# Kernel tuning notes

Hardware: AMD Instinct MI355X
Metric: run time of the kernel (lower is better)

The kernel has to match this reference:

```python
import jax, jax.numpy as jnp
import numpy as np

N = 100000   # nodes
E = 1600000  # edges per snapshot
S = 4        # snapshots
D = 128      # node_dim
H = 256      # hidden dim
P = 10000    # post nodes


def setup_inputs() -> dict:
    key = jax.random.key(0)
    ks = jax.random.split(key, 11)
    return {
        "node_features": jax.random.normal(ks[0], (N, D), jnp.float32),
        "edge_index": jax.random.randint(ks[1], (S, 2, E), 0, N, dtype=jnp.int32),
        "post_idx": jax.random.randint(ks[2], (P,), 0, N, dtype=jnp.int32),
        "W1": jax.random.normal(ks[3], (D, H), jnp.float32) * (1.0 / np.sqrt(D)),
        "b1": jnp.zeros((H,), jnp.float32),
        "W2": jax.random.normal(ks[4], (H, H), jnp.float32) * (1.0 / np.sqrt(H)),
        "b2": jnp.zeros((H,), jnp.float32),
        "Wc1": jax.random.normal(ks[5], (H, H // 2), jnp.float32) * (1.0 / np.sqrt(H)),
        "bc1": jnp.zeros((H // 2,), jnp.float32),
        "Wc2": jax.random.normal(ks[6], (H // 2, 1), jnp.float32) * (1.0 / np.sqrt(H // 2)),
        "bc2": jnp.zeros((1,), jnp.float32),
    }


def _gcn_conv(x, W, b, src, dst):
    # PyG GCNConv: linear transform, then symmetric-normalized aggregation
    # with self-loops: out_i = sum_j (xW)_j / sqrt(d_i d_j) + (xW)_i / d_i + b
    xw = x @ W                                   # [N, H]
    deg = jnp.ones((N,), xw.dtype).at[dst].add(1.0)  # in-degree + self-loop
    dinv = jax.lax.rsqrt(deg)                    # [N]
    norm = dinv[src] * dinv[dst]                 # [E]
    msg = xw[src] * norm[:, None]                # [E, H] gather + scale
    agg = jax.ops.segment_sum(msg, dst, num_segments=N)  # scatter-add
    agg = agg + xw * (dinv * dinv)[:, None]      # self-loop term
    return agg + b


def reference(node_features, edge_index, post_idx, W1, b1, W2, b2, Wc1, bc1, Wc2, bc2):
    embs = []
    for s in range(S):  # small fixed snapshot loop
        src, dst = edge_index[s, 0], edge_index[s, 1]
        # layer 0: 128->256, relu (dropout identity in eval), no residual (dim change)
        h = jax.nn.relu(_gcn_conv(node_features, W1, b1, src, dst))
        # layer 1 (last): no relu, residual since dims match
        h = _gcn_conv(h, W2, b2, src, dst) + h
        embs.append(h)
    agg = jnp.mean(jnp.stack(embs), axis=0)      # 'mean' snapshot aggregation
    post = agg[post_idx]                         # [P, H]
    hid = jax.nn.relu(post @ Wc1 + bc1)
    logits = (hid @ Wc2 + bc2)[:, 0]
    return jax.nn.sigmoid(logits)
```

## Files before the change

### kernel.cpp

```cpp
#include <hip/hip_runtime.h>
#include <math.h>

#define N_NODES 100000
#define E_EDGES 1600000
#define S_SNAP  4
#define D_IN    128
#define H_DIM   256
#define P_POST  10000
#define N4 (S_SNAP * N_NODES)
#define E4 (S_SNAP * E_EDGES)
#define NBLK4 ((N4 + 1023) / 1024)
#define NBIN 8
#define BIN_W (N_NODES / NBIN)
#define FILL_CHUNK 2048
#define FILL_NCHUNK ((E4 + FILL_CHUNK - 1) / FILL_CHUNK)

typedef __attribute__((ext_vector_type(8))) short bf16x8;
typedef __attribute__((ext_vector_type(4))) float f32x4;

__device__ __forceinline__ float bf2f(unsigned short u) {
    union { unsigned int i; float f; } v; v.i = ((unsigned int)u) << 16; return v.f;
}
__device__ __forceinline__ unsigned short f2bf(float f) {
    union { float f; unsigned int i; } v; v.f = f;
    unsigned int lsb = (v.i >> 16) & 1u;
    v.i += 0x7fffu + lsb;
    return (unsigned short)(v.i >> 16);
}

__global__ void zero32_kernel(unsigned int* __restrict__ p, int n) {
    int i = blockIdx.x * blockDim.x + threadIdx.x;
    if (i < n) p[i] = 0u;
}

__global__ void hist4_kernel(const int* __restrict__ ei, int* __restrict__ deg4,
        int* __restrict__ slot4) {
    int i = blockIdx.x * 256 + threadIdx.x;
    int s = i / E_EDGES;
    int j = i - s * E_EDGES;
    int d = ei[(size_t)s * 2 * E_EDGES + E_EDGES + j];
    slot4[i] = atomicAdd(&deg4[s * N_NODES + d], 1);
}

__global__ __launch_bounds__(256) void scan_part4_kernel(const int* __restrict__ deg4,
        int* __restrict__ bsum, float* __restrict__ dinv4) {
    __shared__ int red[4];
    int base = blockIdx.x * 1024 + threadIdx.x * 4;
    int4 v = make_int4(0, 0, 0, 0);
    if (base < N4) {
        v = *(const int4*)(deg4 + base);
        dinv4[base + 0] = rsqrtf((float)(v.x + 1));
        dinv4[base + 1] = rsqrtf((float)(v.y + 1));
        dinv4[base + 2] = rsqrtf((float)(v.z + 1));
        dinv4[base + 3] = rsqrtf((float)(v.w + 1));
    }
    int t = v.x + v.y + v.z + v.w;
    #pragma unroll
    for (int off = 32; off > 0; off >>= 1) t += __shfl_down(t, off, 64);
    int wave = threadIdx.x >> 6, lane = threadIdx.x & 63;
    if (lane == 0) red[wave] = t;
    __syncthreads();
    if (threadIdx.x == 0) bsum[blockIdx.x] = red[0] + red[1] + red[2] + red[3];
}

__global__ __launch_bounds__(512) void scan_top_kernel(const int* __restrict__ bsum,
        int* __restrict__ boff) {
    __shared__ int s[512];
    int t = threadIdx.x;
    s[t] = (t < NBLK4) ? bsum[t] : 0;
    __syncthreads();
    for (int off = 1; off < 512; off <<= 1) {
        int v = (t >= off) ? s[t - off] : 0;
        __syncthreads();
        s[t] += v;
        __syncthreads();
    }
    if (t < NBLK4) boff[t] = (t == 0) ? 0 : s[t - 1];
}

__global__ __launch_bounds__(256) void scan_fin4_kernel(const int* __restrict__ deg4,
        const int* __restrict__ boff, int* __restrict__ rowptr4) {
    __shared__ int sh[256];
    int base = blockIdx.x * 1024 + threadIdx.x * 4;
    int4 v = make_int4(0, 0, 0, 0);
    if (base < N4) v = *(const int4*)(deg4 + base);
    int tsum = v.x + v.y + v.z + v.w;
    sh[threadIdx.x] = tsum;
    __syncthreads();
    for (int off = 1; off < 256; off <<= 1) {
        int u = (threadIdx.x >= off) ? sh[threadIdx.x - off] : 0;
        __syncthreads();
        sh[threadIdx.x] += u;
        __syncthreads();
    }
    int excl = boff[blockIdx.x] + sh[threadIdx.x] - tsum;
    if (base < N4) {
        int4 o;
        o.x = excl;
        o.y = excl + v.x;
        o.z = excl + v.x + v.y;
        o.w = excl + v.x + v.y + v.z;
        *(int4*)(rowptr4 + base) = o;
    }
    if (base == 0) rowptr4[N4] = E4;
}

__global__ __launch_bounds__(256) void fill4_kernel(const int* __restrict__ ei,
        const int* __restrict__ slot4, const int* __restrict__ rowptr4,
        int* __restrict__ csrsrc4) {
    int chunk = blockIdx.x >> 3;
    int bin = blockIdx.x & (NBIN - 1);
    int lo = bin * BIN_W, hi = lo + BIN_W;
    int base = chunk * FILL_CHUNK + threadIdx.x;
    #pragma unroll
    for (int k = 0; k < FILL_CHUNK / 256; ++k) {
        int i = base + k * 256;
        if (i < E4) {
            int s = i / E_EDGES;
            int j = i - s * E_EDGES;
            int d = ei[(size_t)s * 2 * E_EDGES + E_EDGES + j];
            if (d >= lo && d < hi) {
                int sc = ei[(size_t)s * 2 * E_EDGES + j];
                csrsrc4[rowptr4[s * N_NODES + d] + slot4[i]] = sc;
            }
        }
    }
}

__global__ __launch_bounds__(256) void gemm_xw1_mfma(const float* __restrict__ A,
        const float* __restrict__ B, unsigned short* __restrict__ C, int M) {
    __shared__ unsigned short As[64][136];
    __shared__ unsigned short Bs[64][136];
    int tid = threadIdx.x;
    int m0 = blockIdx.x * 64, n0 = blockIdx.y * 64;
    {
        int row = tid >> 2, c0 = (tid & 3) * 32;
        int gm = m0 + row;
        #pragma unroll
        for (int i = 0; i < 8; ++i) {
            float4 v = make_float4(0.f, 0.f, 0.f, 0.f);
            if (gm < M) v = *(const float4*)(A + (size_t)gm * D_IN + c0 + i * 4);
            As[row][c0 + i * 4 + 0] = f2bf(v.x);
            As[row][c0 + i * 4 + 1] = f2bf(v.y);
            As[row][c0 + i * 4 + 2] = f2bf(v.z);
            As[row][c0 + i * 4 + 3] = f2bf(v.w);
        }
    }
    {
        int k = tid >> 1, nb = (tid & 1) * 32;
        #pragma unroll
        for (int i = 0; i < 8; ++i) {
            float4 v = *(const float4*)(B + (size_t)k * H_DIM + n0 + nb + i * 4);
            Bs[nb + i * 4 + 0][k] = f2bf(v.x);
            Bs[nb + i * 4 + 1][k] = f2bf(v.y);
            Bs[nb + i * 4 + 2][k] = f2bf(v.z);
            Bs[nb + i * 4 + 3][k] = f2bf(v.w);
        }
    }
    __syncthreads();
    int w = tid >> 6, l = tid & 63;
    int q = l >> 4, mrow = l & 15;
    f32x4 acc[4] = {{0.f,0.f,0.f,0.f},{0.f,0.f,0.f,0.f},{0.f,0.f,0.f,0.f},{0.f,0.f,0.f,0.f}};
    #pragma unroll
    for (int kk = 0; kk < 4; ++kk) {
        bf16x8 a = *(const bf16x8*)&As[16 * w + mrow][kk * 32 + q * 8];
        #pragma unroll
        for (int ct = 0; ct < 4; ++ct) {
            bf16x8 b = *(const bf16x8*)&Bs[ct * 16 + mrow][kk * 32 + q * 8];
            acc[ct] = __builtin_amdgcn_mfma_f32_16x16x32_bf16(a, b, acc[ct], 0, 0, 0);
        }
    }
    #pragma unroll
    for (int ct = 0; ct < 4; ++ct) {
        int col = n0 + ct * 16 + mrow;
        #pragma unroll
        for (int i = 0; i < 4; ++i) {
            int m = m0 + 16 * w + q * 4 + i;
            if (m < M) C[(size_t)m * H_DIM + col] = f2bf(acc[ct][i]);
        }
    }
}

__global__ __launch_bounds__(256) void spmm_l0_kernel(const unsigned short* __restrict__ xw1,
        const float* __restrict__ dinv4, const int* __restrict__ rowptr4,
        const int* __restrict__ csrsrc4, const float* __restrict__ b1,
        unsigned short* __restrict__ h, int soff) {
    int r = (blockIdx.x << 2) + (threadIdx.x >> 6);
    int lane = threadIdx.x & 63;
    int rg = soff + r;
    int e0 = rowptr4[rg], e1 = rowptr4[rg + 1];
    float di = dinv4[rg];
    float4 acc = make_float4(0.f, 0.f, 0.f, 0.f);
    const ushort4* tp = (const ushort4*)xw1;
    const float* dv = dinv4 + soff;
    int e = e0;
    for (; e + 4 <= e1; e += 4) {
        int s0 = csrsrc4[e], s1 = csrsrc4[e + 1], s2 = csrsrc4[e + 2], s3 = csrsrc4[e + 3];
        float w0 = dv[s0] * di, w1 = dv[s1] * di, w2 = dv[s2] * di, w3 = dv[s3] * di;
        ushort4 u0 = tp[(size_t)s0 * 64 + lane];
        ushort4 u1 = tp[(size_t)s1 * 64 + lane];
        ushort4 u2 = tp[(size_t)s2 * 64 + lane];
        ushort4 u3 = tp[(size_t)s3 * 64 + lane];
        acc.x = fmaf(bf2f(u0.x), w0, acc.x); acc.y = fmaf(bf2f(u0.y), w0, acc.y);
        acc.z = fmaf(bf2f(u0.z), w0, acc.z); acc.w = fmaf(bf2f(u0.w), w0, acc.w);
        acc.x = fmaf(bf2f(u1.x), w1, acc.x); acc.y = fmaf(bf2f(u1.y), w1, acc.y);
        acc.z = fmaf(bf2f(u1.z), w1, acc.z); acc.w = fmaf(bf2f(u1.w), w1, acc.w);
        acc.x = fmaf(bf2f(u2.x), w2, acc.x); acc.y = fmaf(bf2f(u2.y), w2, acc.y);
        acc.z = fmaf(bf2f(u2.z), w2, acc.z); acc.w = fmaf(bf2f(u2.w), w2, acc.w);
        acc.x = fmaf(bf2f(u3.x), w3, acc.x); acc.y = fmaf(bf2f(u3.y), w3, acc.y);
        acc.z = fmaf(bf2f(u3.z), w3, acc.z); acc.w = fmaf(bf2f(u3.w), w3, acc.w);
    }
    for (; e < e1; ++e) {
        int s = csrsrc4[e];
        float wv = dv[s] * di;
        ushort4 u = tp[(size_t)s * 64 + lane];
        acc.x = fmaf(bf2f(u.x), wv, acc.x); acc.y = fmaf(bf2f(u.y), wv, acc.y);
        acc.z = fmaf(bf2f(u.z), wv, acc.z); acc.w = fmaf(bf2f(u.w), wv, acc.w);
    }
    ushort4 us = tp[(size_t)r * 64 + lane];
    float wd = di * di;
    float4 bb = ((const float4*)b1)[lane];
    ushort4 o;
    o.x = f2bf(fmaxf(fmaf(bf2f(us.x), wd, acc.x) + bb.x, 0.f));
    o.y = f2bf(fmaxf(fmaf(bf2f(us.y), wd, acc.y) + bb.y, 0.f));
    o.z = f2bf(fmaxf(fmaf(bf2f(us.z), wd, acc.z) + bb.z, 0.f));
    o.w = f2bf(fmaxf(fmaf(bf2f(us.w), wd, acc.w) + bb.w, 0.f));
    ((ushort4*)h)[(size_t)r * 64 + lane] = o;
}

__global__ __launch_bounds__(256) void spmm_h_post_kernel(const unsigned short* __restrict__ h,
        const float* __restrict__ dinv4, const int* __restrict__ rowptr4,
        const int* __restrict__ csrsrc4, const int* __restrict__ post,
        float* __restrict__ t1p, int soff) {
    int p = (blockIdx.x << 2) + (threadIdx.x >> 6);
    int lane = threadIdx.x & 63;
    int r = post[p];
    int rg = soff + r;
    int e0 = rowptr4[rg], e1 = rowptr4[rg + 1];
    float di = dinv4[rg];
    float4 acc = make_float4(0.f, 0.f, 0.f, 0.f);
    const ushort4* hp = (const ushort4*)h;
    const float* dv = dinv4 + soff;
    int e = e0;
    for (; e + 4 <= e1; e += 4) {
        int s0 = csrsrc4[e], s1 = csrsrc4[e + 1], s2 = csrsrc4[e + 2], s3 = csrsrc4[e + 3];
        float w0 = dv[s0] * di, w1 = dv[s1] * di, w2 = dv[s2] * di, w3 = dv[s3] * di;
        ushort4 u0 = hp[(size_t)s0 * 64 + lane];
        ushort4 u1 = hp[(size_t)s1 * 64 + lane];
        ushort4 u2 = hp[(size_t)s2 * 64 + lane];
        ushort4 u3 = hp[(size_t)s3 * 64 + lane];
        acc.x = fmaf(bf2f(u0.x), w0, acc.x); acc.y = fmaf(bf2f(u0.y), w0, acc.y);
        acc.z = fmaf(bf2f(u0.z), w0, acc.z); acc.w = fmaf(bf2f(u0.w), w0, acc.w);
        acc.x = fmaf(bf2f(u1.x), w1, acc.x); acc.y = fmaf(bf2f(u1.y), w1, acc.y);
        acc.z = fmaf(bf2f(u1.z), w1, acc.z); acc.w = fmaf(bf2f(u1.w), w1, acc.w);
        acc.x = fmaf(bf2f(u2.x), w2, acc.x); acc.y = fmaf(bf2f(u2.y), w2, acc.y);
        acc.z = fmaf(bf2f(u2.z), w2, acc.z); acc.w = fmaf(bf2f(u2.w), w2, acc.w);
        acc.x = fmaf(bf2f(u3.x), w3, acc.x); acc.y = fmaf(bf2f(u3.y), w3, acc.y);
        acc.z = fmaf(bf2f(u3.z), w3, acc.z); acc.w = fmaf(bf2f(u3.w), w3, acc.w);
    }
    for (; e < e1; ++e) {
        int s = csrsrc4[e];
        float wv = dv[s] * di;
        ushort4 u = hp[(size_t)s * 64 + lane];
        acc.x = fmaf(bf2f(u.x), wv, acc.x); acc.y = fmaf(bf2f(u.y), wv, acc.y);
        acc.z = fmaf(bf2f(u.z), wv, acc.z); acc.w = fmaf(bf2f(u.w), wv, acc.w);
    }
    ushort4 u = hp[(size_t)r * 64 + lane];
    float wd = di * di;
    acc.x = fmaf(bf2f(u.x), wd, acc.x);
    acc.y = fmaf(bf2f(u.y), wd, acc.y);
    acc.z = fmaf(bf2f(u.z), wd, acc.z);
    acc.w = fmaf(bf2f(u.w), wd, acc.w);
    ((float4*)t1p)[(size_t)p * 64 + lane] = acc;
}

__global__ __launch_bounds__(256) void gemm_l1_mfma(const float* __restrict__ A,
        const float* __restrict__ B, const float* __restrict__ b2,
        const unsigned short* __restrict__ h, const int* __restrict__ post,
        float* __restrict__ accP, int M) {
    __shared__ unsigned short As[64][136];
    __shared__ unsigned short Bs[64][136];
    int tid = threadIdx.x;
    int m0 = blockIdx.x * 64, n0 = blockIdx.y * 64;
    int w = tid >> 6, l = tid & 63;
    int q = l >> 4, mrow = l & 15;
    f32x4 acc[4] = {{0.f,0.f,0.f,0.f},{0.f,0.f,0.f,0.f},{0.f,0.f,0.f,0.f},{0.f,0.f,0.f,0.f}};
    for (int kk = 0; kk < 256; kk += 128) {
        __syncthreads();
        {
            int row = tid >> 2, c0 = (tid & 3) * 32;
            int gm = m0 + row;
            #pragma unroll
            for (int i = 0; i < 8; ++i) {
                float4 v = make_float4(0.f, 0.f, 0.f, 0.f);
                if (gm < M) v = *(const float4*)(A + (size_t)gm * 256 + kk + c0 + i * 4);
                As[row][c0 + i * 4 + 0] = f2bf(v.x);
                As[row][c0 + i * 4 + 1] = f2bf(v.y);
                As[row][c0 + i * 4 + 2] = f2bf(v.z);
                As[row][c0 + i * 4 + 3] = f2bf(v.w);
            }
        }
        {
            int k = tid >> 1, nb = (tid & 1) * 32;
            #pragma unroll
            for (int i = 0; i < 8; ++i) {
                float4 v = *(const float4*)(B + (size_t)(kk + k) * H_DIM + n0 + nb + i * 4);
                Bs[nb + i * 4 + 0][k] = f2bf(v.x);
                Bs[nb + i * 4 + 1][k] = f2bf(v.y);
                Bs[nb + i * 4 + 2][k] = f2bf(v.z);
                Bs[nb + i * 4 + 3][k] = f2bf(v.w);
            }
        }
        __syncthreads();
        #pragma unroll
        for (int ks = 0; ks < 4; ++ks) {
            bf16x8 a = *(const bf16x8*)&As[16 * w + mrow][ks * 32 + q * 8];
            #pragma unroll
            for (int ct = 0; ct < 4; ++ct) {
                bf16x8 b = *(const bf16x8*)&Bs[ct * 16 + mrow][ks * 32 + q * 8];
                acc[ct] = __builtin_amdgcn_mfma_f32_16x16x32_bf16(a, b, acc[ct], 0, 0, 0);
            }
        }
    }
    #pragma unroll
    for (int ct = 0; ct < 4; ++ct) {
        int col = n0 + ct * 16 + mrow;
        float bias = b2[col];
        #pragma unroll
        for (int i = 0; i < 4; ++i) {
            int m = m0 + 16 * w + q * 4 + i;
            if (m < M) {
                int node = post[m];
                float hv = bf2f(h[(size_t)node * 256 + col]);
                accP[(size_t)m * 256 + col] += acc[ct][i] + bias + hv;
            }
        }
    }
}

__global__ __launch_bounds__(128) void classifier_kernel(const float* __restrict__ accP,
        const float* __restrict__ Wc1, const float* __restrict__ bc1,
        const float* __restrict__ Wc2, const float* __restrict__ bc2,
        float* __restrict__ out) {
    __shared__ float arow[8][256];
    __shared__ float red[2][8];
    int p0 = blockIdx.x << 3;
    int tid = threadIdx.x;
    for (int idx = tid; idx < 8 * 256; idx += 128) {
        int pl = idx >> 8, k = idx & 255;
        arow[pl][k] = 0.25f * accP[(size_t)(p0 + pl) * 256 + k];
    }
    __syncthreads();
    float s[8];
    float b = bc1[tid];
    #pragma unroll
    for (int pl = 0; pl < 8; ++pl) s[pl] = b;
    for (int k = 0; k < 256; ++k) {
        float wv = Wc1[k * 128 + tid];
        #pragma unroll
        for (int pl = 0; pl < 8; ++pl) s[pl] = fmaf(arow[pl][k], wv, s[pl]);
    }
    float wc2 = Wc2[tid];
    float part[8];
    #pragma unroll
    for (int pl = 0; pl < 8; ++pl) part[pl] = fmaxf(s[pl], 0.f) * wc2;
    #pragma unroll
    for (int off = 32; off > 0; off >>= 1)
        #pragma unroll
        for (int pl = 0; pl < 8; ++pl) part[pl] += __shfl_down(part[pl], off, 64);
    int wave = tid >> 6, lane = tid & 63;
    if (lane == 0) {
        #pragma unroll
        for (int pl = 0; pl < 8; ++pl) red[wave][pl] = part[pl];
    }
    __syncthreads();
    if (tid < 8) {
        float logit = red[0][tid] + red[1][tid] + bc2[0];
        out[p0 + tid] = 1.f / (1.f + expf(-logit));
    }
}

extern "C" void kernel_launch(void* const* d_in, const int* in_sizes, int n_in,
                              void* d_out, int out_size, void* d_ws, size_t ws_size,
                              hipStream_t stream) {
    const float* x   = (const float*)d_in[0];
    const int*   ei  = (const int*)d_in[1];
    const int*   post= (const int*)d_in[2];
    const float* W1  = (const float*)d_in[3];
    const float* b1  = (const float*)d_in[4];
    const float* W2  = (const float*)d_in[5];
    const float* b2  = (const float*)d_in[6];
    const float* Wc1 = (const float*)d_in[7];
    const float* bc1 = (const float*)d_in[8];
    const float* Wc2 = (const float*)d_in[9];
    const float* bc2 = (const float*)d_in[10];
    float* out = (float*)d_out;

    char* w = (char*)d_ws;
    size_t off = 0;
#define WS_ALLOC(type, name, count) \
    type* name = (type*)(w + off); \
    off += (((size_t)(count) * sizeof(type)) + 255) & ~(size_t)255;
    WS_ALLOC(unsigned short, xw1,     (size_t)N_NODES * H_DIM)
    WS_ALLOC(unsigned short, hbuf,    (size_t)N_NODES * H_DIM)
    WS_ALLOC(float,          t1p,     (size_t)P_POST * H_DIM)
    WS_ALLOC(float,          accP,    (size_t)P_POST * H_DIM)
    WS_ALLOC(int,            deg4,    N4)
    WS_ALLOC(float,          dinv4,   N4)
    WS_ALLOC(int,            rowptr4, N4 + 4)
    WS_ALLOC(int,            csrsrc4, E4)
    WS_ALLOC(int,            bsum,    NBLK4)
    WS_ALLOC(int,            boff,    NBLK4)
#undef WS_ALLOC
    int* slot4 = (int*)hbuf;
    (void)ws_size; (void)in_sizes; (void)n_in; (void)out_size;

    zero32_kernel<<<(P_POST * H_DIM + N4 + 255) / 256, 256, 0, stream>>>(
        (unsigned int*)accP, P_POST * H_DIM + N4);

    hist4_kernel<<<E4 / 256, 256, 0, stream>>>(ei, deg4, slot4);
    scan_part4_kernel<<<NBLK4, 256, 0, stream>>>(deg4, bsum, dinv4);
    scan_top_kernel<<<1, 512, 0, stream>>>(bsum, boff);
    scan_fin4_kernel<<<NBLK4, 256, 0, stream>>>(deg4, boff, rowptr4);
    fill4_kernel<<<FILL_NCHUNK * NBIN, 256, 0, stream>>>(ei, slot4, rowptr4, csrsrc4);

    dim3 gg((N_NODES + 63) / 64, H_DIM / 64);
    gemm_xw1_mfma<<<gg, 256, 0, stream>>>(x, W1, xw1, N_NODES);

    for (int s = 0; s < S_SNAP; ++s) {
        int soff = s * N_NODES;
        spmm_l0_kernel<<<N_NODES / 4, 256, 0, stream>>>(xw1, dinv4, rowptr4, csrsrc4,
                                                        b1, hbuf, soff);
        spmm_h_post_kernel<<<P_POST / 4, 256, 0, stream>>>(hbuf, dinv4, rowptr4, csrsrc4,
                                                           post, t1p, soff);
        dim3 g1((P_POST + 63) / 64, H_DIM / 64);
        gemm_l1_mfma<<<g1, 256, 0, stream>>>(t1p, W2, b2, hbuf, post, accP, P_POST);
    }
    classifier_kernel<<<P_POST / 8, 128, 0, stream>>>(accP, Wc1, bc1, Wc2, bc2, out);
}
```

Before: 1.295 ms.

## Build CSR with per-bin LDS histograms and chunk prefix instead of global atomics

Replaces the global-atomic degree histogram and per-edge slot array with block-local shared-memory counting per (snapshot, destination bin, edge chunk), followed by a per-row prefix over chunks to produce degrees and chunk offsets. The fill kernel then recomputes local slots with LDS atomics and writes source ids at rowptr + chunk offset + local slot. The aim is to remove contended global atomics and the slot array traffic. In exchange, each block rescans its whole edge chunk for every bin (8x more reads of dst), and CSR order within a row is no longer deterministic.

```diff
diff --git a/kernel.cpp b/kernel.cpp
--- a/kernel.cpp
+++ b/kernel.cpp
@@ -12,8 +12,10 @@
 #define NBLK4 ((N4 + 1023) / 1024)
 #define NBIN 8
 #define BIN_W (N_NODES / NBIN)
-#define FILL_CHUNK 2048
-#define FILL_NCHUNK ((E4 + FILL_CHUNK - 1) / FILL_CHUNK)
+#define C_CHUNK 16
+#define EPC (E_EDGES / C_CHUNK)
+#define PREP_BLOCKS (S_SNAP * NBIN * C_CHUNK)
+#define ROWS_PER_BLK (BIN_W / 4)
 
 typedef __attribute__((ext_vector_type(8))) short bf16x8;
 typedef __attribute__((ext_vector_type(4))) float f32x4;
@@ -33,13 +35,46 @@
     if (i < n) p[i] = 0u;
 }
 
-__global__ void hist4_kernel(const int* __restrict__ ei, int* __restrict__ deg4,
-        int* __restrict__ slot4) {
-    int i = blockIdx.x * 256 + threadIdx.x;
-    int s = i / E_EDGES;
-    int j = i - s * E_EDGES;
-    int d = ei[(size_t)s * 2 * E_EDGES + E_EDGES + j];
-    slot4[i] = atomicAdd(&deg4[s * N_NODES + d], 1);
+__global__ __launch_bounds__(256) void count_kernel(const int* __restrict__ ei,
+        int* __restrict__ counts) {
+    __shared__ int cnt[BIN_W];
+    for (int r = threadIdx.x; r < BIN_W; r += 256) cnt[r] = 0;
+    __syncthreads();
+    int bx = blockIdx.x;
+    int c = bx & (C_CHUNK - 1);
+    int b = (bx >> 4) & (NBIN - 1);
+    int s = bx >> 7;
+    int lo = b * BIN_W;
+    const int* dstp = ei + (size_t)s * 2 * E_EDGES + E_EDGES;
+    int j1 = (c + 1) * EPC;
+    for (int j = c * EPC + threadIdx.x; j < j1; j += 256) {
+        int d = dstp[j] - lo;
+        if ((unsigned)d < BIN_W) atomicAdd(&cnt[d], 1);
+    }
+    __syncthreads();
+    int* outp = counts + (size_t)bx * BIN_W;
+    for (int r = threadIdx.x; r < BIN_W; r += 256) outp[r] = cnt[r];
+}
+
+__global__ __launch_bounds__(256) void chunkprefix_kernel(int* __restrict__ counts,
+        int* __restrict__ deg4) {
+    int bx = blockIdx.x;
+    int rc = bx & 3;
+    int b = (bx >> 2) & (NBIN - 1);
+    int s = bx >> 5;
+    size_t base = ((size_t)(s * NBIN + b) * C_CHUNK) * BIN_W;
+    int r1 = (rc + 1) * ROWS_PER_BLK;
+    for (int r = rc * ROWS_PER_BLK + threadIdx.x; r < r1; r += 256) {
+        int run = 0;
+        #pragma unroll
+        for (int c = 0; c < C_CHUNK; ++c) {
+            size_t idx = base + (size_t)c * BIN_W + r;
+            int v = counts[idx];
+            counts[idx] = run;
+            run += v;
+        }
+        deg4[s * N_NODES + b * BIN_W + r] = run;
+    }
 }
 
 __global__ __launch_bounds__(256) void scan_part4_kernel(const int* __restrict__ deg4,
@@ -105,24 +140,27 @@
     if (base == 0) rowptr4[N4] = E4;
 }
 
-__global__ __launch_bounds__(256) void fill4_kernel(const int* __restrict__ ei,
-        const int* __restrict__ slot4, const int* __restrict__ rowptr4,
+__global__ __launch_bounds__(256) void fillb_kernel(const int* __restrict__ ei,
+        const int* __restrict__ counts, const int* __restrict__ rowptr4,
         int* __restrict__ csrsrc4) {
-    int chunk = blockIdx.x >> 3;
-    int bin = blockIdx.x & (NBIN - 1);
-    int lo = bin * BIN_W, hi = lo + BIN_W;
-    int base = chunk * FILL_CHUNK + threadIdx.x;
-    #pragma unroll
-    for (int k = 0; k < FILL_CHUNK / 256; ++k) {
-        int i = base + k * 256;
-        if (i < E4) {
-            int s = i / E_EDGES;
-            int j = i - s * E_EDGES;
-            int d = ei[(size_t)s * 2 * E_EDGES + E_EDGES + j];
-            if (d >= lo && d < hi) {
-                int sc = ei[(size_t)s * 2 * E_EDGES + j];
-                csrsrc4[rowptr4[s * N_NODES + d] + slot4[i]] = sc;
-            }
+    __shared__ int cnt[BIN_W];
+    for (int r = threadIdx.x; r < BIN_W; r += 256) cnt[r] = 0;
+    __syncthreads();
+    int bx = blockIdx.x;
+    int c = bx & (C_CHUNK - 1);
+    int b = (bx >> 4) & (NBIN - 1);
+    int s = bx >> 7;
+    int lo = b * BIN_W;
+    const int* srcp = ei + (size_t)s * 2 * E_EDGES;
+    const int* dstp = srcp + E_EDGES;
+    const int* cb = counts + (size_t)bx * BIN_W;
+    const int* rp = rowptr4 + s * N_NODES + lo;
+    int j1 = (c + 1) * EPC;
+    for (int j = c * EPC + threadIdx.x; j < j1; j += 256) {
+        int d = dstp[j] - lo;
+        if ((unsigned)d < BIN_W) {
+            int ls = atomicAdd(&cnt[d], 1);
+            csrsrc4[rp[d] + cb[d] + ls] = srcp[j];
         }
     }
 }
@@ -412,17 +450,18 @@
     WS_ALLOC(int,            bsum,    NBLK4)
     WS_ALLOC(int,            boff,    NBLK4)
 #undef WS_ALLOC
-    int* slot4 = (int*)hbuf;
+    int* counts = (int*)hbuf;
     (void)ws_size; (void)in_sizes; (void)n_in; (void)out_size;
 
-    zero32_kernel<<<(P_POST * H_DIM + N4 + 255) / 256, 256, 0, stream>>>(
-        (unsigned int*)accP, P_POST * H_DIM + N4);
-
-    hist4_kernel<<<E4 / 256, 256, 0, stream>>>(ei, deg4, slot4);
+    zero32_kernel<<<(P_POST * H_DIM + 255) / 256, 256, 0, stream>>>(
+        (unsigned int*)accP, P_POST * H_DIM);
+
+    count_kernel<<<PREP_BLOCKS, 256, 0, stream>>>(ei, counts);
+    chunkprefix_kernel<<<S_SNAP * NBIN * 4, 256, 0, stream>>>(counts, deg4);
     scan_part4_kernel<<<NBLK4, 256, 0, stream>>>(deg4, bsum, dinv4);
     scan_top_kernel<<<1, 512, 0, stream>>>(bsum, boff);
     scan_fin4_kernel<<<NBLK4, 256, 0, stream>>>(deg4, boff, rowptr4);
-    fill4_kernel<<<FILL_NCHUNK * NBIN, 256, 0, stream>>>(ei, slot4, rowptr4, csrsrc4);
+    fillb_kernel<<<PREP_BLOCKS, 256, 0, stream>>>(ei, counts, rowptr4, csrsrc4);
 
     dim3 gg((N_NODES + 63) / 64, H_DIM / 64);
     gemm_xw1_mfma<<<gg, 256, 0, stream>>>(x, W1, xw1, N_NODES);
```

Result: slower. 1.477 ms (+14.1%).
